# Optimization experiments

Hardware: AMD Instinct MI355X
Metric: run time of the kernel (lower is better)

The kernel has to match this reference:

```python
import jax, jax.numpy as jnp
import numpy as np
from jax import lax

NUM_HEADS = 8
EPS = 1e-12  # torch F.normalize default eps


def setup_inputs() -> dict:
    key = jax.random.key(0)
    ks = jax.random.split(key, 5)
    b, c, h, w = 8, 128, 128, 128
    return {
        "x_in": jax.random.normal(ks[0], (b, c, h, w), dtype=jnp.float32),
        "illu_fea": jax.random.normal(ks[1], (b, c, h, w), dtype=jnp.float32),
        "w_qkv": jax.random.normal(ks[2], (3 * c, c), dtype=jnp.float32) * 0.05,
        "w_dw": jax.random.normal(ks[3], (3 * c, 1, 3, 3), dtype=jnp.float32) * 0.2,
        "w_proj": jax.random.normal(ks[4], (c, c), dtype=jnp.float32) * 0.05,
        "temperature": jnp.ones((NUM_HEADS, 1, 1), dtype=jnp.float32),
    }


def _l2norm(t):
    # F.normalize(t, dim=-1, p=2): t / max(||t||_2, eps)
    n = jnp.sqrt(jnp.sum(t * t, axis=-1, keepdims=True))
    return t / jnp.maximum(n, EPS)


def reference(x_in, illu_fea, w_qkv, w_dw, w_proj, temperature):
    b, c, h, w = x_in.shape
    dh = c // NUM_HEADS
    # 1x1 conv (pointwise channel GEMM): [b,c,h,w] -> [b,3c,h,w]
    qkv = jnp.einsum("bchw,oc->bohw", x_in, w_qkv)
    # depthwise 3x3 conv, groups = 3c, SAME padding
    qkv = lax.conv_general_dilated(
        qkv, w_dw, window_strides=(1, 1), padding="SAME",
        dimension_numbers=("NCHW", "OIHW", "NCHW"),
        feature_group_count=3 * c,
    )
    q, k, v = jnp.split(qkv, 3, axis=1)
    # b (head dh) h w -> b head dh (h*w)
    rs = lambda t: t.reshape(b, NUM_HEADS, dh, h * w)
    q, k, v = rs(q), rs(k), rs(v)
    v = v * illu_fea.reshape(b, NUM_HEADS, dh, h * w)  # illumination gating
    q = _l2norm(q)
    k = _l2norm(k)
    # channel-wise attention: [b,head,dh,dh], contract over spatial N = h*w
    attn = jnp.einsum("bhcn,bhdn->bhcd", q, k) * temperature
    attn = jax.nn.softmax(attn, axis=-1)
    out = jnp.einsum("bhcd,bhdn->bhcn", attn, v).reshape(b, c, h, w)
    out = jnp.einsum("bchw,oc->bohw", out, w_proj)  # project_out 1x1 conv
    return out
```

## Files before the change

kernel.cpp:

```cpp
#include <hip/hip_runtime.h>
#include <hip/hip_bf16.h>

typedef __attribute__((ext_vector_type(8))) short bf16x8;
typedef __attribute__((ext_vector_type(4))) float f32x4;

__device__ __forceinline__ unsigned short f2b(float f) {
    unsigned int u = __builtin_bit_cast(unsigned int, f);
    u += 0x7FFFu + ((u >> 16) & 1u);
    return (unsigned short)(u >> 16);
}
__device__ __forceinline__ float b2f(unsigned short h) {
    unsigned int u = ((unsigned int)h) << 16;
    return __builtin_bit_cast(float, u);
}

#define OFFB_QKV1 0L
#define OFFB_DWQK 100663296L
#define OFFB_VGT  167772160L
#define OFFB_WBF  201326592L
#define OFFB_G    201424896L
#define OFFB_NQK  201490432L
#define OFFB_ATTN 201498624L
#define OFFB_CTB  201564160L

__global__ __launch_bounds__(256) void prep_w(const float* __restrict__ w,
                                              unsigned short* __restrict__ wbf)
{
    int e = blockIdx.x * 256 + threadIdx.x;
    float4 v = *(const float4*)&w[e * 4];
    unsigned int p0 = (unsigned int)f2b(v.x) | ((unsigned int)f2b(v.y) << 16);
    unsigned int p1 = (unsigned int)f2b(v.z) | ((unsigned int)f2b(v.w) << 16);
    *(uint2*)&wbf[e * 4] = make_uint2(p0, p1);
}

__global__ __launch_bounds__(256) void transpose_cb(const float* __restrict__ in,
                                                    unsigned short* __restrict__ out)
{
    const int b  = blockIdx.z;
    const int c0 = blockIdx.y * 32;
    const int n0 = blockIdx.x * 64;
    __shared__ float s[32][65];
    const int tid = threadIdx.x;
    const float* ib = in + ((long)b * 128 + c0) * 16384 + n0;
#pragma unroll
    for (int i = 0; i < 2; ++i) {
        int e = tid + i * 256;
        int c = e >> 4, n4 = (e & 15) * 4;
        *(float4*)&s[c][n4] = *(const float4*)&ib[(long)c * 16384 + n4];
    }
    __syncthreads();
    const int n = tid >> 2, cg = (tid & 3) * 8;
    unsigned int p[4];
#pragma unroll
    for (int j = 0; j < 4; ++j)
        p[j] = (unsigned int)f2b(s[cg + 2*j][n]) | ((unsigned int)f2b(s[cg + 2*j + 1][n]) << 16);
    *(uint4*)&out[((long)b * 16384 + n0 + n) * 128 + c0 + cg] = make_uint4(p[0], p[1], p[2], p[3]);
}

__global__ __launch_bounds__(256) void transpose_vg(const unsigned short* __restrict__ in,
                                                    unsigned short* __restrict__ out)
{
    const int b  = blockIdx.z;
    const int c0 = blockIdx.y * 32;
    const int n0 = blockIdx.x * 64;
    __shared__ float s[32][65];
    const int tid = threadIdx.x;
    const unsigned short* ib = in + ((long)b * 128 + c0) * 16384 + n0;
    {
        int c = tid >> 3, ng = (tid & 7) * 8;
        uint4 v = *(const uint4*)&ib[(long)c * 16384 + ng];
        unsigned int uu[4] = {v.x, v.y, v.z, v.w};
#pragma unroll
        for (int j = 0; j < 4; ++j) {
            s[c][ng + 2*j]     = __builtin_bit_cast(float, uu[j] << 16);
            s[c][ng + 2*j + 1] = __builtin_bit_cast(float, uu[j] & 0xFFFF0000u);
        }
    }
    __syncthreads();
    const int n = tid >> 2, cg = (tid & 3) * 8;
    unsigned int p[4];
#pragma unroll
    for (int j = 0; j < 4; ++j)
        p[j] = (unsigned int)f2b(s[cg + 2*j][n]) | ((unsigned int)f2b(s[cg + 2*j + 1][n]) << 16);
    *(uint4*)&out[((long)b * 16384 + n0 + n) * 128 + c0 + cg] = make_uint4(p[0], p[1], p[2], p[3]);
}

template<int OUT_BF16>
__global__ __launch_bounds__(256) void mfma_gemm(
    const unsigned short* __restrict__ A, long aBatch,
    const unsigned short* __restrict__ Bt, void* __restrict__ Cv, int M)
{
    const int b  = blockIdx.z;
    const int m0 = blockIdx.y * 128;
    const int n0 = blockIdx.x * 128;
    const unsigned short* Ab = A  + (long)b * aBatch + (long)m0 * 128;
    const unsigned short* Bb = Bt + ((long)b * 16384 + n0) * 128;

    __shared__ unsigned short As[128][136];
    __shared__ unsigned short Bs[128][136];

    const int tid = threadIdx.x;
#pragma unroll
    for (int i = 0; i < 8; ++i) {
        int ch = tid + i * 256;
        int row = ch >> 4, cg = (ch & 15) * 8;
        *(uint4*)&As[row][cg] = *(const uint4*)&Ab[row * 128 + cg];
        *(uint4*)&Bs[row][cg] = *(const uint4*)&Bb[row * 128 + cg];
    }
    __syncthreads();

    const int l  = tid & 63;
    const int w  = tid >> 6;
    const int mb = (w & 1) * 64, nb = (w >> 1) * 64;
    const int lr = l & 15, lg = l >> 4;

    f32x4 acc[4][4];
    const f32x4 zero = {0.f, 0.f, 0.f, 0.f};
#pragma unroll
    for (int mi = 0; mi < 4; ++mi)
#pragma unroll
        for (int ni = 0; ni < 4; ++ni) acc[mi][ni] = zero;

#pragma unroll
    for (int kk = 0; kk < 128; kk += 32) {
        bf16x8 af[4], bfr[4];
#pragma unroll
        for (int mi = 0; mi < 4; ++mi)
            af[mi] = *(const bf16x8*)&As[mb + mi * 16 + lr][kk + lg * 8];
#pragma unroll
        for (int ni = 0; ni < 4; ++ni)
            bfr[ni] = *(const bf16x8*)&Bs[nb + ni * 16 + lr][kk + lg * 8];
#pragma unroll
        for (int mi = 0; mi < 4; ++mi)
#pragma unroll
            for (int ni = 0; ni < 4; ++ni)
                acc[mi][ni] = __builtin_amdgcn_mfma_f32_16x16x32_bf16(
                    af[mi], bfr[ni], acc[mi][ni], 0, 0, 0);
    }

    if (OUT_BF16) {
        __syncthreads();
        unsigned short* ct = &As[0][0];
#pragma unroll
        for (int mi = 0; mi < 4; ++mi)
#pragma unroll
            for (int ni = 0; ni < 4; ++ni)
#pragma unroll
                for (int r = 0; r < 4; ++r)
                    ct[(mb + mi * 16 + lg * 4 + r) * 128 + nb + ni * 16 + lr] =
                        f2b(acc[mi][ni][r]);
        __syncthreads();
        unsigned short* Cg = (unsigned short*)Cv + ((long)b * M + m0) * 16384 + n0;
#pragma unroll
        for (int i = 0; i < 8; ++i) {
            int ch = tid + i * 256;
            int row = ch >> 4, cg = (ch & 15) * 8;
            *(uint4*)&Cg[(long)row * 16384 + cg] = *(const uint4*)&ct[row * 128 + cg];
        }
    } else {
        float* Cg = (float*)Cv + ((long)b * M + m0) * 16384 + n0;
#pragma unroll
        for (int mi = 0; mi < 4; ++mi)
#pragma unroll
            for (int ni = 0; ni < 4; ++ni)
#pragma unroll
                for (int r = 0; r < 4; ++r)
                    Cg[(long)(mb + mi * 16 + lg * 4 + r) * 16384 + nb + ni * 16 + lr] =
                        acc[mi][ni][r];
    }
}

__global__ __launch_bounds__(256) void dw_norm_gate(
    const unsigned short* __restrict__ qkv1, const float* __restrict__ wdw,
    const float* __restrict__ illu, unsigned short* __restrict__ Vg,
    unsigned short* __restrict__ dwqk, float* __restrict__ nqk)
{
    const int b = blockIdx.z, ch = blockIdx.y;
    const int y0 = blockIdx.x * 16;
    const int tid = threadIdx.x;
    __shared__ float lds[18][136];
    __shared__ float wsum[4];
    const unsigned short* in = qkv1 + ((long)b * 384 + ch) * 16384;

    float wv[9];
#pragma unroll
    for (int j = 0; j < 9; ++j) wv[j] = wdw[ch * 9 + j];

#pragma unroll
    for (int i = 0; i < 2; ++i) {
        int chk = tid + i * 256;
        if (chk < 288) {
            int row = chk >> 4, xg = (chk & 15) * 8;
            int yy = y0 + row - 1;
            float f[8];
            if (yy >= 0 && yy < 128) {
                uint4 v = *(const uint4*)&in[yy * 128 + xg];
                unsigned int uu[4] = {v.x, v.y, v.z, v.w};
#pragma unroll
                for (int j = 0; j < 4; ++j) {
                    f[2*j]   = __builtin_bit_cast(float, uu[j] << 16);
                    f[2*j+1] = __builtin_bit_cast(float, uu[j] & 0xFFFF0000u);
                }
            } else {
#pragma unroll
                for (int j = 0; j < 8; ++j) f[j] = 0.f;
            }
            *(float4*)&lds[row][xg + 4] = make_float4(f[0], f[1], f[2], f[3]);
            *(float4*)&lds[row][xg + 8] = make_float4(f[4], f[5], f[6], f[7]);
        }
    }
    if (tid < 18) lds[tid][3] = 0.f;
    else if (tid < 50 && tid >= 32) lds[tid - 32][132] = 0.f;
    __syncthreads();

    const int x  = tid & 127;
    const int rt = (tid >> 7) * 8;
    float c0[10], c1[10], c2[10];
#pragma unroll
    for (int t = 0; t < 10; ++t) {
        c0[t] = lds[rt + t][x + 3];
        c1[t] = lds[rt + t][x + 4];
        c2[t] = lds[rt + t][x + 5];
    }
    float o[8];
#pragma unroll
    for (int rr = 0; rr < 8; ++rr) {
        float a = 0.f;
        a = fmaf(wv[0], c0[rr],     a); a = fmaf(wv[1], c1[rr],     a); a = fmaf(wv[2], c2[rr],     a);
        a = fmaf(wv[3], c0[rr + 1], a); a = fmaf(wv[4], c1[rr + 1], a); a = fmaf(wv[5], c2[rr + 1], a);
        a = fmaf(wv[6], c0[rr + 2], a); a = fmaf(wv[7], c1[rr + 2], a); a = fmaf(wv[8], c2[rr + 2], a);
        o[rr] = a;
    }

    if (ch >= 256) {
        const int c = ch - 256;
        const float* ib = illu + ((long)b * 128 + c) * 16384 + y0 * 128;
        unsigned short* ob = Vg + ((long)b * 128 + c) * 16384 + y0 * 128;
#pragma unroll
        for (int rr = 0; rr < 8; ++rr) {
            int ry = rt + rr;
            ob[ry * 128 + x] = f2b(o[rr] * ib[ry * 128 + x]);
        }
    } else {
        unsigned short* db = dwqk + ((long)b * 256 + ch) * 16384 + y0 * 128;
        float s = 0.f;
#pragma unroll
        for (int rr = 0; rr < 8; ++rr) {
            int ry = rt + rr;
            unsigned short h = f2b(o[rr]);
            db[ry * 128 + x] = h;
            float f = b2f(h);
            s = fmaf(f, f, s);
        }
#pragma unroll
        for (int off = 32; off > 0; off >>= 1) s += __shfl_down(s, off);
        if ((tid & 63) == 0) wsum[tid >> 6] = s;
        __syncthreads();
        if (tid == 0) atomicAdd(&nqk[b * 256 + ch], wsum[0] + wsum[1] + wsum[2] + wsum[3]);
    }
}

__global__ __launch_bounds__(256) void gram_mfma(const unsigned short* __restrict__ dwqk,
                                                 float* __restrict__ G)
{
    const int hd = blockIdx.y, b = blockIdx.z;
    const int tid = threadIdx.x;
    const int l = tid & 63, w = tid >> 6;
    const int lr = l & 15, lg = l >> 4;
    const unsigned short* qb = dwqk + ((long)b * 256 + hd * 16) * 16384;
    const unsigned short* kb = dwqk + ((long)b * 256 + 128 + hd * 16) * 16384;
    const int n0 = blockIdx.x * 1024 + w * 256;

    f32x4 acc = {0.f, 0.f, 0.f, 0.f};
#pragma unroll
    for (int ks = 0; ks < 8; ++ks) {
        const int n = n0 + ks * 32 + lg * 8;
        bf16x8 a = *(const bf16x8*)&qb[(long)lr * 16384 + n];
        bf16x8 bb = *(const bf16x8*)&kb[(long)lr * 16384 + n];
        acc = __builtin_amdgcn_mfma_f32_16x16x32_bf16(a, bb, acc, 0, 0, 0);
    }

    __shared__ float sg[4][16][16];
#pragma unroll
    for (int r = 0; r < 4; ++r) sg[w][lg * 4 + r][lr] = acc[r];
    __syncthreads();
    const int row = tid >> 4, col = tid & 15;
    float v = sg[0][row][col] + sg[1][row][col] + sg[2][row][col] + sg[3][row][col];
    atomicAdd(&G[(((long)b * 8 + hd) * 16 + row) * 16 + col], v);
}

__global__ void softmax_attn(const float* __restrict__ G, const float* __restrict__ nqk,
                             const float* __restrict__ temp, float* __restrict__ attn)
{
    const int hd = blockIdx.x, b = blockIdx.y;
    const int r = threadIdx.x;
    if (r >= 16) return;
    const float tv = temp[hd];
    const float* g = G + ((long)(b * 8 + hd) * 16 + r) * 16;
    float mq = fmaxf(sqrtf(nqk[b * 256 + hd * 16 + r]), 1e-12f);
    float L[16];
    float mx = -1e30f;
#pragma unroll
    for (int d = 0; d < 16; ++d) {
        float mk = fmaxf(sqrtf(nqk[b * 256 + 128 + hd * 16 + d]), 1e-12f);
        L[d] = g[d] * tv / (mq * mk);
        mx = fmaxf(mx, L[d]);
    }
    float s = 0.f;
#pragma unroll
    for (int d = 0; d < 16; ++d) { L[d] = expf(L[d] - mx); s += L[d]; }
    float inv = 1.f / s;
    float* arow = attn + ((long)(b * 8 + hd) * 16 + r) * 16;
#pragma unroll
    for (int d = 0; d < 16; ++d) arow[d] = L[d] * inv;
}

__global__ __launch_bounds__(256) void compose_kernel(
    const float* __restrict__ wproj, const float* __restrict__ attn,
    unsigned short* __restrict__ CtBo)
{
    const int b = blockIdx.x, tid = threadIdx.x;
#pragma unroll 1
    for (int e = tid; e < 16384; e += 256) {
        const int o = e >> 7, D = e & 127;
        const int hd = D >> 4, d = D & 15;
        const float* ar = attn + (long)(b * 8 + hd) * 256 + d;
        const float* wr = wproj + o * 128 + hd * 16;
        float s = 0.f;
#pragma unroll
        for (int c2 = 0; c2 < 16; ++c2) s = fmaf(wr[c2], ar[c2 * 16], s);
        CtBo[((long)b * 128 + o) * 128 + D] = f2b(s);
    }
}

extern "C" void kernel_launch(void* const* d_in, const int* in_sizes, int n_in,
                              void* d_out, int out_size, void* d_ws, size_t ws_size,
                              hipStream_t stream)
{
    const float* x     = (const float*)d_in[0];
    const float* illu  = (const float*)d_in[1];
    const float* wqkv  = (const float*)d_in[2];
    const float* wdw   = (const float*)d_in[3];
    const float* wproj = (const float*)d_in[4];
    const float* temp  = (const float*)d_in[5];
    float* out = (float*)d_out;
    char*  wsb = (char*)d_ws;

    unsigned short* qkv1 = (unsigned short*)(wsb + OFFB_QKV1);
    unsigned short* dwqk = (unsigned short*)(wsb + OFFB_DWQK);
    unsigned short* xT   = dwqk;
    unsigned short* VgT  = (unsigned short*)(wsb + OFFB_VGT);
    unsigned short* wbf  = (unsigned short*)(wsb + OFFB_WBF);
    float* G    = (float*)(wsb + OFFB_G);
    float* nqk  = (float*)(wsb + OFFB_NQK);
    float* attn = (float*)(wsb + OFFB_ATTN);
    unsigned short* CtBo = (unsigned short*)(wsb + OFFB_CTB);
    unsigned short* Vg   = (unsigned short*)d_out;

    hipLaunchKernelGGL(prep_w, dim3(48), dim3(256), 0, stream, wqkv, wbf);
    hipMemsetAsync(G, 0, 73728, stream);
    hipLaunchKernelGGL(transpose_cb, dim3(256, 4, 8), dim3(256), 0, stream, x, xT);
    hipLaunchKernelGGL(HIP_KERNEL_NAME(mfma_gemm<1>), dim3(128, 3, 8), dim3(256), 0, stream,
                       wbf, 0L, xT, (void*)qkv1, 384);
    hipLaunchKernelGGL(dw_norm_gate, dim3(8, 384, 8), dim3(256), 0, stream,
                       qkv1, wdw, illu, Vg, dwqk, nqk);
    hipLaunchKernelGGL(gram_mfma, dim3(16, 8, 8), dim3(256), 0, stream, dwqk, G);
    hipLaunchKernelGGL(softmax_attn, dim3(8, 8), dim3(64), 0, stream, G, nqk, temp, attn);
    hipLaunchKernelGGL(compose_kernel, dim3(8), dim3(256), 0, stream, wproj, attn, CtBo);
    hipLaunchKernelGGL(transpose_vg, dim3(256, 4, 8), dim3(256), 0, stream, Vg, VgT);
    hipLaunchKernelGGL(HIP_KERNEL_NAME(mfma_gemm<0>), dim3(128, 1, 8), dim3(256), 0, stream,
                       CtBo, 16384L, VgT, (void*)out, 128);
}
```

Measured before the change: 292.6 us.

## Fuse depthwise q/k conv into Gram MFMA and V transpose into output GEMM

The depthwise 3x3 conv for q/k is computed directly inside the Gram kernel. Each block stages a strip of qkv1 in LDS, runs the conv, and feeds the bf16 results straight into MFMA while also accumulating the squared norms. This removes the dwqk intermediate write and read-back. The V transpose moves into the final projection GEMM through an LDS staging buffer, and softmax is merged with compose while the G zeroing moves into the weight-prep kernel. Together these cut a large amount of global traffic and several launches, at the cost of more complex kernels with halo re-reads, a transposed LDS layout that may cause bank conflicts, and a serialized transpose loop before the final GEMM.

```diff
diff --git a/kernel.cpp b/kernel.cpp
--- a/kernel.cpp
+++ b/kernel.cpp
@@ -15,22 +15,25 @@
 }
 
 #define OFFB_QKV1 0L
-#define OFFB_DWQK 100663296L
-#define OFFB_VGT  167772160L
+#define OFFB_SLOT2 100663296L
 #define OFFB_WBF  201326592L
 #define OFFB_G    201424896L
 #define OFFB_NQK  201490432L
-#define OFFB_ATTN 201498624L
 #define OFFB_CTB  201564160L
 
-__global__ __launch_bounds__(256) void prep_w(const float* __restrict__ w,
-                                              unsigned short* __restrict__ wbf)
-{
-    int e = blockIdx.x * 256 + threadIdx.x;
-    float4 v = *(const float4*)&w[e * 4];
-    unsigned int p0 = (unsigned int)f2b(v.x) | ((unsigned int)f2b(v.y) << 16);
-    unsigned int p1 = (unsigned int)f2b(v.z) | ((unsigned int)f2b(v.w) << 16);
-    *(uint2*)&wbf[e * 4] = make_uint2(p0, p1);
+__global__ __launch_bounds__(256) void prep_w_zero(const float* __restrict__ w,
+                                                   unsigned short* __restrict__ wbf,
+                                                   float* __restrict__ Gz)
+{
+    if (blockIdx.x < 48) {
+        int e = blockIdx.x * 256 + threadIdx.x;
+        float4 v = *(const float4*)&w[e * 4];
+        unsigned int p0 = (unsigned int)f2b(v.x) | ((unsigned int)f2b(v.y) << 16);
+        unsigned int p1 = (unsigned int)f2b(v.z) | ((unsigned int)f2b(v.w) << 16);
+        *(uint2*)&wbf[e * 4] = make_uint2(p0, p1);
+    } else {
+        for (int i = threadIdx.x; i < 18432; i += 256) Gz[i] = 0.f;
+    }
 }
 
 __global__ __launch_bounds__(256) void transpose_cb(const float* __restrict__ in,
@@ -57,43 +60,14 @@
     *(uint4*)&out[((long)b * 16384 + n0 + n) * 128 + c0 + cg] = make_uint4(p[0], p[1], p[2], p[3]);
 }
 
-__global__ __launch_bounds__(256) void transpose_vg(const unsigned short* __restrict__ in,
-                                                    unsigned short* __restrict__ out)
-{
-    const int b  = blockIdx.z;
-    const int c0 = blockIdx.y * 32;
-    const int n0 = blockIdx.x * 64;
-    __shared__ float s[32][65];
-    const int tid = threadIdx.x;
-    const unsigned short* ib = in + ((long)b * 128 + c0) * 16384 + n0;
-    {
-        int c = tid >> 3, ng = (tid & 7) * 8;
-        uint4 v = *(const uint4*)&ib[(long)c * 16384 + ng];
-        unsigned int uu[4] = {v.x, v.y, v.z, v.w};
-#pragma unroll
-        for (int j = 0; j < 4; ++j) {
-            s[c][ng + 2*j]     = __builtin_bit_cast(float, uu[j] << 16);
-            s[c][ng + 2*j + 1] = __builtin_bit_cast(float, uu[j] & 0xFFFF0000u);
-        }
-    }
-    __syncthreads();
-    const int n = tid >> 2, cg = (tid & 3) * 8;
-    unsigned int p[4];
-#pragma unroll
-    for (int j = 0; j < 4; ++j)
-        p[j] = (unsigned int)f2b(s[cg + 2*j][n]) | ((unsigned int)f2b(s[cg + 2*j + 1][n]) << 16);
-    *(uint4*)&out[((long)b * 16384 + n0 + n) * 128 + c0 + cg] = make_uint4(p[0], p[1], p[2], p[3]);
-}
-
-template<int OUT_BF16>
-__global__ __launch_bounds__(256) void mfma_gemm(
-    const unsigned short* __restrict__ A, long aBatch,
-    const unsigned short* __restrict__ Bt, void* __restrict__ Cv, int M)
+__global__ __launch_bounds__(256) void mfma_gemm_k1(
+    const unsigned short* __restrict__ A,
+    const unsigned short* __restrict__ Bt, unsigned short* __restrict__ C)
 {
     const int b  = blockIdx.z;
     const int m0 = blockIdx.y * 128;
     const int n0 = blockIdx.x * 128;
-    const unsigned short* Ab = A  + (long)b * aBatch + (long)m0 * 128;
+    const unsigned short* Ab = A + (long)m0 * 128;
     const unsigned short* Bb = Bt + ((long)b * 16384 + n0) * 128;
 
     __shared__ unsigned short As[128][136];
@@ -138,48 +112,132 @@
                     af[mi], bfr[ni], acc[mi][ni], 0, 0, 0);
     }
 
-    if (OUT_BF16) {
+    __syncthreads();
+    unsigned short* ct = &As[0][0];
+#pragma unroll
+    for (int mi = 0; mi < 4; ++mi)
+#pragma unroll
+        for (int ni = 0; ni < 4; ++ni)
+#pragma unroll
+            for (int r = 0; r < 4; ++r)
+                ct[(mb + mi * 16 + lg * 4 + r) * 128 + nb + ni * 16 + lr] =
+                    f2b(acc[mi][ni][r]);
+    __syncthreads();
+    unsigned short* Cg = C + ((long)b * 384 + m0) * 16384 + n0;
+#pragma unroll
+    for (int i = 0; i < 8; ++i) {
+        int ch = tid + i * 256;
+        int row = ch >> 4, cg = (ch & 15) * 8;
+        *(uint4*)&Cg[(long)row * 16384 + cg] = *(const uint4*)&ct[row * 128 + cg];
+    }
+}
+
+__global__ __launch_bounds__(256) void dw_qk_gram(
+    const unsigned short* __restrict__ qkv1, const float* __restrict__ wdw,
+    float* __restrict__ G, float* __restrict__ nqk)
+{
+    const int strip = blockIdx.x, hd = blockIdx.y, b = blockIdx.z;
+    const int y0 = strip * 8;
+    const int tid = threadIdx.x;
+    const int l = tid & 63, w = tid >> 6;
+    const int lr = l & 15, lg = l >> 4;
+
+    __shared__ unsigned short st[10][130][18];
+    __shared__ float sg[4][16][16];
+
+    if (tid < 180) {
+        int y = tid / 18, c = tid - y * 18;
+        st[y][0][c] = 0; st[y][129][c] = 0;
+    }
+
+    const int sch = tid & 15;
+    const int sxc = tid >> 4;
+
+    bf16x8 af[8];
+    f32x4 acc = {0.f, 0.f, 0.f, 0.f};
+    float qn = 0.f, kn = 0.f;
+
+    for (int op = 0; op < 2; ++op) {
+        const int chbase = op * 128 + hd * 16;
         __syncthreads();
-        unsigned short* ct = &As[0][0];
-#pragma unroll
-        for (int mi = 0; mi < 4; ++mi)
-#pragma unroll
-            for (int ni = 0; ni < 4; ++ni)
-#pragma unroll
-                for (int r = 0; r < 4; ++r)
-                    ct[(mb + mi * 16 + lg * 4 + r) * 128 + nb + ni * 16 + lr] =
-                        f2b(acc[mi][ni][r]);
+        const unsigned short* src = qkv1 + ((long)b * 384 + chbase + sch) * 16384;
+#pragma unroll
+        for (int y = 0; y < 10; ++y) {
+            int yy = y0 + y - 1;
+            uint4 v = make_uint4(0, 0, 0, 0);
+            if (yy >= 0 && yy < 128) v = *(const uint4*)&src[yy * 128 + sxc * 8];
+            unsigned short* d = &st[y][sxc * 8 + 1][sch];
+            d[0]   = (unsigned short)(v.x);
+            d[18]  = (unsigned short)(v.x >> 16);
+            d[36]  = (unsigned short)(v.y);
+            d[54]  = (unsigned short)(v.y >> 16);
+            d[72]  = (unsigned short)(v.z);
+            d[90]  = (unsigned short)(v.z >> 16);
+            d[108] = (unsigned short)(v.w);
+            d[126] = (unsigned short)(v.w >> 16);
+        }
         __syncthreads();
-        unsigned short* Cg = (unsigned short*)Cv + ((long)b * M + m0) * 16384 + n0;
-#pragma unroll
-        for (int i = 0; i < 8; ++i) {
-            int ch = tid + i * 256;
-            int row = ch >> 4, cg = (ch & 15) * 8;
-            *(uint4*)&Cg[(long)row * 16384 + cg] = *(const uint4*)&ct[row * 128 + cg];
-        }
-    } else {
-        float* Cg = (float*)Cv + ((long)b * M + m0) * 16384 + n0;
-#pragma unroll
-        for (int mi = 0; mi < 4; ++mi)
-#pragma unroll
-            for (int ni = 0; ni < 4; ++ni)
-#pragma unroll
-                for (int r = 0; r < 4; ++r)
-                    Cg[(long)(mb + mi * 16 + lg * 4 + r) * 16384 + nb + ni * 16 + lr] =
-                        acc[mi][ni][r];
-    }
-}
-
-__global__ __launch_bounds__(256) void dw_norm_gate(
+
+        float wv[9];
+#pragma unroll
+        for (int j = 0; j < 9; ++j) wv[j] = wdw[(chbase + lr) * 9 + j];
+
+#pragma unroll
+        for (int j = 0; j < 8; ++j) {
+            const int yb = 2 * w + (j >> 2);
+            const int x0 = (j & 3) * 32 + lg * 8;
+            float r0[10], r1[10], r2[10];
+#pragma unroll
+            for (int i = 0; i < 10; ++i) {
+                r0[i] = b2f(st[yb][x0 + i][lr]);
+                r1[i] = b2f(st[yb + 1][x0 + i][lr]);
+                r2[i] = b2f(st[yb + 2][x0 + i][lr]);
+            }
+            bf16x8 fr;
+            float nrm = 0.f;
+#pragma unroll
+            for (int i = 0; i < 8; ++i) {
+                float a = 0.f;
+                a = fmaf(wv[0], r0[i], a); a = fmaf(wv[1], r0[i+1], a); a = fmaf(wv[2], r0[i+2], a);
+                a = fmaf(wv[3], r1[i], a); a = fmaf(wv[4], r1[i+1], a); a = fmaf(wv[5], r1[i+2], a);
+                a = fmaf(wv[6], r2[i], a); a = fmaf(wv[7], r2[i+1], a); a = fmaf(wv[8], r2[i+2], a);
+                unsigned short hh = f2b(a);
+                fr[i] = (short)hh;
+                float f = b2f(hh);
+                nrm = fmaf(f, f, nrm);
+            }
+            if (op == 0) { af[j] = fr; qn += nrm; }
+            else {
+                kn += nrm;
+                acc = __builtin_amdgcn_mfma_f32_16x16x32_bf16(af[j], fr, acc, 0, 0, 0);
+            }
+        }
+    }
+
+    qn += __shfl_xor(qn, 16); qn += __shfl_xor(qn, 32);
+    kn += __shfl_xor(kn, 16); kn += __shfl_xor(kn, 32);
+    if (l < 16) {
+        atomicAdd(&nqk[b * 256 + hd * 16 + lr], qn);
+        atomicAdd(&nqk[b * 256 + 128 + hd * 16 + lr], kn);
+    }
+
+#pragma unroll
+    for (int r = 0; r < 4; ++r) sg[w][lg * 4 + r][lr] = acc[r];
+    __syncthreads();
+    const int row = tid >> 4, col = tid & 15;
+    float v = sg[0][row][col] + sg[1][row][col] + sg[2][row][col] + sg[3][row][col];
+    atomicAdd(&G[(((long)b * 8 + hd) * 16 + row) * 16 + col], v);
+}
+
+__global__ __launch_bounds__(256) void dw_v_gate(
     const unsigned short* __restrict__ qkv1, const float* __restrict__ wdw,
-    const float* __restrict__ illu, unsigned short* __restrict__ Vg,
-    unsigned short* __restrict__ dwqk, float* __restrict__ nqk)
-{
-    const int b = blockIdx.z, ch = blockIdx.y;
+    const float* __restrict__ illu, unsigned short* __restrict__ Vg)
+{
+    const int b = blockIdx.z, c = blockIdx.y;
+    const int ch = 256 + c;
     const int y0 = blockIdx.x * 16;
     const int tid = threadIdx.x;
     __shared__ float lds[18][136];
-    __shared__ float wsum[4];
     const unsigned short* in = qkv1 + ((long)b * 384 + ch) * 16384;
 
     float wv[9];
@@ -222,115 +280,143 @@
         c1[t] = lds[rt + t][x + 4];
         c2[t] = lds[rt + t][x + 5];
     }
-    float o[8];
+    const float* ib = illu + ((long)b * 128 + c) * 16384 + y0 * 128;
+    unsigned short* ob = Vg + ((long)b * 128 + c) * 16384 + y0 * 128;
 #pragma unroll
     for (int rr = 0; rr < 8; ++rr) {
         float a = 0.f;
         a = fmaf(wv[0], c0[rr],     a); a = fmaf(wv[1], c1[rr],     a); a = fmaf(wv[2], c2[rr],     a);
         a = fmaf(wv[3], c0[rr + 1], a); a = fmaf(wv[4], c1[rr + 1], a); a = fmaf(wv[5], c2[rr + 1], a);
         a = fmaf(wv[6], c0[rr + 2], a); a = fmaf(wv[7], c1[rr + 2], a); a = fmaf(wv[8], c2[rr + 2], a);
-        o[rr] = a;
-    }
-
-    if (ch >= 256) {
-        const int c = ch - 256;
-        const float* ib = illu + ((long)b * 128 + c) * 16384 + y0 * 128;
-        unsigned short* ob = Vg + ((long)b * 128 + c) * 16384 + y0 * 128;
-#pragma unroll
-        for (int rr = 0; rr < 8; ++rr) {
-            int ry = rt + rr;
-            ob[ry * 128 + x] = f2b(o[rr] * ib[ry * 128 + x]);
-        }
-    } else {
-        unsigned short* db = dwqk + ((long)b * 256 + ch) * 16384 + y0 * 128;
+        int ry = rt + rr;
+        ob[ry * 128 + x] = f2b(a * ib[ry * 128 + x]);
+    }
+}
+
+__global__ __launch_bounds__(256) void softmax_compose(
+    const float* __restrict__ G, const float* __restrict__ nqk,
+    const float* __restrict__ temp, const float* __restrict__ wproj,
+    unsigned short* __restrict__ CtBo)
+{
+    const int b = blockIdx.x;
+    const int tid = threadIdx.x;
+    __shared__ float sa[8][16][16];
+    if (tid < 128) {
+        const int hd = tid >> 4, r = tid & 15;
+        const float tv = temp[hd];
+        const float* g = G + ((long)(b * 8 + hd) * 16 + r) * 16;
+        float mq = fmaxf(sqrtf(nqk[b * 256 + hd * 16 + r]), 1e-12f);
+        float L[16];
+        float mx = -1e30f;
+#pragma unroll
+        for (int d = 0; d < 16; ++d) {
+            float mk = fmaxf(sqrtf(nqk[b * 256 + 128 + hd * 16 + d]), 1e-12f);
+            L[d] = g[d] * tv / (mq * mk);
+            mx = fmaxf(mx, L[d]);
+        }
         float s = 0.f;
 #pragma unroll
-        for (int rr = 0; rr < 8; ++rr) {
-            int ry = rt + rr;
-            unsigned short h = f2b(o[rr]);
-            db[ry * 128 + x] = h;
-            float f = b2f(h);
-            s = fmaf(f, f, s);
-        }
-#pragma unroll
-        for (int off = 32; off > 0; off >>= 1) s += __shfl_down(s, off);
-        if ((tid & 63) == 0) wsum[tid >> 6] = s;
-        __syncthreads();
-        if (tid == 0) atomicAdd(&nqk[b * 256 + ch], wsum[0] + wsum[1] + wsum[2] + wsum[3]);
-    }
-}
-
-__global__ __launch_bounds__(256) void gram_mfma(const unsigned short* __restrict__ dwqk,
-                                                 float* __restrict__ G)
-{
-    const int hd = blockIdx.y, b = blockIdx.z;
-    const int tid = threadIdx.x;
-    const int l = tid & 63, w = tid >> 6;
-    const int lr = l & 15, lg = l >> 4;
-    const unsigned short* qb = dwqk + ((long)b * 256 + hd * 16) * 16384;
-    const unsigned short* kb = dwqk + ((long)b * 256 + 128 + hd * 16) * 16384;
-    const int n0 = blockIdx.x * 1024 + w * 256;
-
-    f32x4 acc = {0.f, 0.f, 0.f, 0.f};
-#pragma unroll
-    for (int ks = 0; ks < 8; ++ks) {
-        const int n = n0 + ks * 32 + lg * 8;
-        bf16x8 a = *(const bf16x8*)&qb[(long)lr * 16384 + n];
-        bf16x8 bb = *(const bf16x8*)&kb[(long)lr * 16384 + n];
-        acc = __builtin_amdgcn_mfma_f32_16x16x32_bf16(a, bb, acc, 0, 0, 0);
-    }
-
-    __shared__ float sg[4][16][16];
-#pragma unroll
-    for (int r = 0; r < 4; ++r) sg[w][lg * 4 + r][lr] = acc[r];
-    __syncthreads();
-    const int row = tid >> 4, col = tid & 15;
-    float v = sg[0][row][col] + sg[1][row][col] + sg[2][row][col] + sg[3][row][col];
-    atomicAdd(&G[(((long)b * 8 + hd) * 16 + row) * 16 + col], v);
-}
-
-__global__ void softmax_attn(const float* __restrict__ G, const float* __restrict__ nqk,
-                             const float* __restrict__ temp, float* __restrict__ attn)
-{
-    const int hd = blockIdx.x, b = blockIdx.y;
-    const int r = threadIdx.x;
-    if (r >= 16) return;
-    const float tv = temp[hd];
-    const float* g = G + ((long)(b * 8 + hd) * 16 + r) * 16;
-    float mq = fmaxf(sqrtf(nqk[b * 256 + hd * 16 + r]), 1e-12f);
-    float L[16];
-    float mx = -1e30f;
-#pragma unroll
-    for (int d = 0; d < 16; ++d) {
-        float mk = fmaxf(sqrtf(nqk[b * 256 + 128 + hd * 16 + d]), 1e-12f);
-        L[d] = g[d] * tv / (mq * mk);
-        mx = fmaxf(mx, L[d]);
-    }
-    float s = 0.f;
-#pragma unroll
-    for (int d = 0; d < 16; ++d) { L[d] = expf(L[d] - mx); s += L[d]; }
-    float inv = 1.f / s;
-    float* arow = attn + ((long)(b * 8 + hd) * 16 + r) * 16;
-#pragma unroll
-    for (int d = 0; d < 16; ++d) arow[d] = L[d] * inv;
-}
-
-__global__ __launch_bounds__(256) void compose_kernel(
-    const float* __restrict__ wproj, const float* __restrict__ attn,
-    unsigned short* __restrict__ CtBo)
-{
-    const int b = blockIdx.x, tid = threadIdx.x;
+        for (int d = 0; d < 16; ++d) { L[d] = expf(L[d] - mx); s += L[d]; }
+        float inv = 1.f / s;
+#pragma unroll
+        for (int d = 0; d < 16; ++d) sa[hd][r][d] = L[d] * inv;
+    }
+    __syncthreads();
 #pragma unroll 1
     for (int e = tid; e < 16384; e += 256) {
         const int o = e >> 7, D = e & 127;
-        const int hd = D >> 4, d = D & 15;
-        const float* ar = attn + (long)(b * 8 + hd) * 256 + d;
-        const float* wr = wproj + o * 128 + hd * 16;
+        const int hd2 = D >> 4, d = D & 15;
+        const float* wr = wproj + o * 128 + hd2 * 16;
         float s = 0.f;
 #pragma unroll
-        for (int c2 = 0; c2 < 16; ++c2) s = fmaf(wr[c2], ar[c2 * 16], s);
+        for (int c2 = 0; c2 < 16; ++c2) s = fmaf(wr[c2], sa[hd2][c2][d], s);
         CtBo[((long)b * 128 + o) * 128 + D] = f2b(s);
     }
+}
+
+__global__ __launch_bounds__(256) void mfma_k6(
+    const unsigned short* __restrict__ CtBo, const unsigned short* __restrict__ Vg,
+    float* __restrict__ out)
+{
+    const int b  = blockIdx.y;
+    const int n0 = blockIdx.x * 128;
+    __shared__ unsigned short As[128][136];
+    __shared__ unsigned short Bs[128][136];
+    __shared__ float sfl[32][65];
+    const int tid = threadIdx.x;
+
+    const unsigned short* Ab = CtBo + (long)b * 16384;
+#pragma unroll
+    for (int i = 0; i < 8; ++i) {
+        int ch = tid + i * 256;
+        int row = ch >> 4, cg = (ch & 15) * 8;
+        *(uint4*)&As[row][cg] = *(const uint4*)&Ab[row * 128 + cg];
+    }
+
+    const unsigned short* Vb = Vg + (long)b * 128 * 16384;
+#pragma unroll 1
+    for (int it = 0; it < 8; ++it) {
+        const int c0 = (it & 3) * 32, nb0 = (it >> 2) * 64;
+        {
+            int c = tid >> 3, n8 = (tid & 7) * 8;
+            uint4 v = *(const uint4*)&Vb[(long)(c0 + c) * 16384 + n0 + nb0 + n8];
+            unsigned int uu[4] = {v.x, v.y, v.z, v.w};
+#pragma unroll
+            for (int j = 0; j < 4; ++j) {
+                sfl[c][n8 + 2*j]     = __builtin_bit_cast(float, uu[j] << 16);
+                sfl[c][n8 + 2*j + 1] = __builtin_bit_cast(float, uu[j] & 0xFFFF0000u);
+            }
+        }
+        __syncthreads();
+        {
+            int n = tid >> 2, cg = (tid & 3) * 8;
+            unsigned int p[4];
+#pragma unroll
+            for (int j = 0; j < 4; ++j)
+                p[j] = (unsigned int)f2b(sfl[cg + 2*j][n]) | ((unsigned int)f2b(sfl[cg + 2*j + 1][n]) << 16);
+            *(uint4*)&Bs[nb0 + n][c0 + cg] = make_uint4(p[0], p[1], p[2], p[3]);
+        }
+        __syncthreads();
+    }
+
+    const int l  = tid & 63;
+    const int w  = tid >> 6;
+    const int mb = (w & 1) * 64, nb = (w >> 1) * 64;
+    const int lr = l & 15, lg = l >> 4;
+
+    f32x4 acc[4][4];
+    const f32x4 zero = {0.f, 0.f, 0.f, 0.f};
+#pragma unroll
+    for (int mi = 0; mi < 4; ++mi)
+#pragma unroll
+        for (int ni = 0; ni < 4; ++ni) acc[mi][ni] = zero;
+
+#pragma unroll
+    for (int kk = 0; kk < 128; kk += 32) {
+        bf16x8 af[4], bfr[4];
+#pragma unroll
+        for (int mi = 0; mi < 4; ++mi)
+            af[mi] = *(const bf16x8*)&As[mb + mi * 16 + lr][kk + lg * 8];
+#pragma unroll
+        for (int ni = 0; ni < 4; ++ni)
+            bfr[ni] = *(const bf16x8*)&Bs[nb + ni * 16 + lr][kk + lg * 8];
+#pragma unroll
+        for (int mi = 0; mi < 4; ++mi)
+#pragma unroll
+            for (int ni = 0; ni < 4; ++ni)
+                acc[mi][ni] = __builtin_amdgcn_mfma_f32_16x16x32_bf16(
+                    af[mi], bfr[ni], acc[mi][ni], 0, 0, 0);
+    }
+
+    float* Cg = out + ((long)b * 128) * 16384 + n0;
+#pragma unroll
+    for (int mi = 0; mi < 4; ++mi)
+#pragma unroll
+        for (int ni = 0; ni < 4; ++ni)
+#pragma unroll
+            for (int r = 0; r < 4; ++r)
+                Cg[(long)(mb + mi * 16 + lg * 4 + r) * 16384 + nb + ni * 16 + lr] =
+                    acc[mi][ni][r];
 }
 
 extern "C" void kernel_launch(void* const* d_in, const int* in_sizes, int n_in,
@@ -347,27 +433,23 @@
     char*  wsb = (char*)d_ws;
 
     unsigned short* qkv1 = (unsigned short*)(wsb + OFFB_QKV1);
-    unsigned short* dwqk = (unsigned short*)(wsb + OFFB_DWQK);
-    unsigned short* xT   = dwqk;
-    unsigned short* VgT  = (unsigned short*)(wsb + OFFB_VGT);
+    unsigned short* xT   = (unsigned short*)(wsb + OFFB_SLOT2);
+    unsigned short* Vg   = (unsigned short*)(wsb + OFFB_SLOT2);
     unsigned short* wbf  = (unsigned short*)(wsb + OFFB_WBF);
     float* G    = (float*)(wsb + OFFB_G);
     float* nqk  = (float*)(wsb + OFFB_NQK);
-    float* attn = (float*)(wsb + OFFB_ATTN);
     unsigned short* CtBo = (unsigned short*)(wsb + OFFB_CTB);
-    unsigned short* Vg   = (unsigned short*)d_out;
-
-    hipLaunchKernelGGL(prep_w, dim3(48), dim3(256), 0, stream, wqkv, wbf);
-    hipMemsetAsync(G, 0, 73728, stream);
+
+    hipLaunchKernelGGL(prep_w_zero, dim3(49), dim3(256), 0, stream, wqkv, wbf, G);
     hipLaunchKernelGGL(transpose_cb, dim3(256, 4, 8), dim3(256), 0, stream, x, xT);
-    hipLaunchKernelGGL(HIP_KERNEL_NAME(mfma_gemm<1>), dim3(128, 3, 8), dim3(256), 0, stream,
-                       wbf, 0L, xT, (void*)qkv1, 384);
-    hipLaunchKernelGGL(dw_norm_gate, dim3(8, 384, 8), dim3(256), 0, stream,
-                       qkv1, wdw, illu, Vg, dwqk, nqk);
-    hipLaunchKernelGGL(gram_mfma, dim3(16, 8, 8), dim3(256), 0, stream, dwqk, G);
-    hipLaunchKernelGGL(softmax_attn, dim3(8, 8), dim3(64), 0, stream, G, nqk, temp, attn);
-    hipLaunchKernelGGL(compose_kernel, dim3(8), dim3(256), 0, stream, wproj, attn, CtBo);
-    hipLaunchKernelGGL(transpose_vg, dim3(256, 4, 8), dim3(256), 0, stream, Vg, VgT);
-    hipLaunchKernelGGL(HIP_KERNEL_NAME(mfma_gemm<0>), dim3(128, 1, 8), dim3(256), 0, stream,
-                       CtBo, 16384L, VgT, (void*)out, 128);
-}
+    hipLaunchKernelGGL(mfma_gemm_k1, dim3(128, 3, 8), dim3(256), 0, stream,
+                       wbf, xT, qkv1);
+    hipLaunchKernelGGL(dw_v_gate, dim3(8, 128, 8), dim3(256), 0, stream,
+                       qkv1, wdw, illu, Vg);
+    hipLaunchKernelGGL(dw_qk_gram, dim3(16, 8, 8), dim3(256), 0, stream,
+                       qkv1, wdw, G, nqk);
+    hipLaunchKernelGGL(softmax_compose, dim3(8), dim3(256), 0, stream,
+                       G, nqk, temp, wproj, CtBo);
+    hipLaunchKernelGGL(mfma_k6, dim3(128, 8), dim3(256), 0, stream,
+                       CtBo, Vg, out);
+}
```

After: 280.7 us. 4.1% less time.
